# Kernel tuning notes

Hardware: AMD Instinct MI355X
Metric: run time of the kernel (lower is better)

## Reference

```python
import jax, jax.numpy as jnp
import numpy as np

B, T, D = 2, 2048, 1024
N_HEADS, N_KV_HEADS = 16, 4
D_HEAD = D // N_HEADS            # 64
N_GROUPS = N_HEADS // N_KV_HEADS  # 4
ROPE_THETA = 10000.0


def _rope_freqs(t, d_head, theta):
    inv = 1.0 / (theta ** (jnp.arange(0, d_head, 2, dtype=jnp.float32) / d_head))  # (d_head/2,)
    ang = jnp.arange(t, dtype=jnp.float32)[:, None] * inv[None, :]                 # (T, d_head/2)
    return jnp.stack([jnp.cos(ang), jnp.sin(ang)], axis=-1)                        # (T, d_head/2, 2)


def _apply_rope(x, freqs):
    # x: (B, T, H, d_head); freqs: (T, d_head/2, 2) = (cos, sin)
    xr = x.reshape(*x.shape[:-1], -1, 2)          # (B,T,H,d/2,2)
    xre, xim = xr[..., 0], xr[..., 1]
    fre = freqs[None, :, None, :, 0]              # (1,T,1,d/2)
    fim = freqs[None, :, None, :, 1]
    outre = xre * fre - xim * fim
    outim = xre * fim + xim * fre
    return jnp.stack([outre, outim], axis=-1).reshape(x.shape)


def setup_inputs() -> dict:
    key = jax.random.key(0)
    ks = jax.random.split(key, 5)
    x = jax.random.normal(ks[0], (B, T, D), dtype=jnp.float32)
    w_q = jax.random.normal(ks[1], (N_HEADS * D_HEAD, D), dtype=jnp.float32) * 0.02
    w_k = jax.random.normal(ks[2], (N_KV_HEADS * D_HEAD, D), dtype=jnp.float32) * 0.02
    w_v = jax.random.normal(ks[3], (N_KV_HEADS * D_HEAD, D), dtype=jnp.float32) * 0.02
    w_o = jax.random.normal(ks[4], (D, N_HEADS * D_HEAD), dtype=jnp.float32) * 0.02
    rope_freqs = _rope_freqs(T, D_HEAD, ROPE_THETA)
    causal = jnp.tril(jnp.ones((T, T), dtype=bool))
    mask = jnp.where(causal, 0.0, -1e9).astype(jnp.float32)[None, None]  # (1,1,T,T)
    return {"x": x, "rope_freqs": rope_freqs, "mask": mask,
            "w_q": w_q, "w_k": w_k, "w_v": w_v, "w_o": w_o}


def reference(x, rope_freqs, mask, w_q, w_k, w_v, w_o):
    # projections (torch Linear: y = x @ W.T)
    q = jnp.einsum('btd,od->bto', x, w_q).reshape(B, T, N_HEADS, D_HEAD)
    k = jnp.einsum('btd,od->bto', x, w_k).reshape(B, T, N_KV_HEADS, D_HEAD)
    v = jnp.einsum('btd,od->bto', x, w_v).reshape(B, T, N_KV_HEADS, D_HEAD)
    q = _apply_rope(q, rope_freqs)
    k = _apply_rope(k, rope_freqs)
    # GQA: expand KV heads (kv head h -> N_GROUPS contiguous query heads)
    k = jnp.repeat(k, N_GROUPS, axis=2)   # (B,T,H,d)
    v = jnp.repeat(v, N_GROUPS, axis=2)
    q = q.transpose(0, 2, 1, 3)           # (B,H,T,d)
    k = k.transpose(0, 2, 1, 3)
    v = v.transpose(0, 2, 1, 3)
    scale = 1.0 / np.sqrt(D_HEAD).astype(np.float32)
    scores = jnp.einsum('bhqd,bhkd->bhqk', q, k) * scale + mask
    attn = jax.nn.softmax(scores, axis=-1)
    out = jnp.einsum('bhqk,bhkd->bhqd', attn, v)
    out = out.transpose(0, 2, 1, 3).reshape(B, T, N_HEADS * D_HEAD)
    return jnp.einsum('bto,do->btd', out, w_o)
```

## Files before the change

kernel.cpp:

```cpp
#include <hip/hip_runtime.h>
#include <hip/hip_bf16.h>
#include <cstddef>
#include <type_traits>

#define TT   2048
#define NH   16
#define NKV  4
#define DH   64

typedef __bf16 bf16x8 __attribute__((ext_vector_type(8)));
typedef float  f32x4  __attribute__((ext_vector_type(4)));

#if __has_builtin(__builtin_amdgcn_exp2f)
#define EXP2F(x) __builtin_amdgcn_exp2f(x)
#else
#define EXP2F(x) __expf((x) * 0.69314718056f)
#endif

#define QSCALE 0.180336880f

__global__ __launch_bounds__(256)
void cast_kernel(const float* __restrict__ x,  const float* __restrict__ wq,
                 const float* __restrict__ wk, const float* __restrict__ wv,
                 const float* __restrict__ wo,
                 __bf16* __restrict__ xb, __bf16* __restrict__ wqkv,
                 __bf16* __restrict__ wob)
{
    const int g = blockIdx.x * 256 + threadIdx.x;
    const float* src;
    __bf16* dst;
    int off;
    if (g < 1048576)       { src = x;  dst = xb;   off = g; }
    else if (g < 1310720)  { src = wq; dst = wqkv; off = g - 1048576; }
    else if (g < 1376256)  { src = wk; dst = wqkv + 1048576; off = g - 1310720; }
    else if (g < 1441792)  { src = wv; dst = wqkv + 1310720; off = g - 1376256; }
    else                   { src = wo; dst = wob;  off = g - 1441792; }
    const float4 v = *(const float4*)(src + (size_t)off * 4);
    union { __bf16 h[4]; uint2 u; } o;
    o.h[0] = (__bf16)v.x; o.h[1] = (__bf16)v.y;
    o.h[2] = (__bf16)v.z; o.h[3] = (__bf16)v.w;
    *(uint2*)(dst + (size_t)off * 4) = o.u;
}

template<int MODE>
__global__ __launch_bounds__(256, 3)
void mm_kernel(const __bf16* __restrict__ A,
               const __bf16* __restrict__ W,
               const float* __restrict__ rope,
               void* __restrict__ O0, void* __restrict__ O1,
               void* __restrict__ O2)
{
    constexpr int K  = 1024;
    constexpr int NK = K / 32;
    constexpr int NX = (MODE == 0) ? 12 : 8;
    __shared__ __bf16 As[2][64 * 32];
    __shared__ __bf16 Bs[2][128 * 32];

    const int tid  = threadIdx.x;
    const int lane = tid & 63;
    const int wv   = tid >> 6;
    const int quad = lane >> 4;
    const int lc   = lane & 15;

    const int dlin = blockIdx.x + NX * blockIdx.y;
    const int nid  = (dlin & 7) * ((NX * 64) >> 3) + (dlin >> 3);
    const int bx   = nid % NX;
    const int by   = nid / NX;

    const int gm0  = by * 64;
    const int gn0  = bx * 128;
    const int wc0  = wv * 32;

    size_t gaA;  int lsA;
    {
        const int p = tid;
        const int r = p >> 2, q = (p & 3) ^ ((r >> 1) & 3);
        gaA = (size_t)r * K + q * 8;
        lsA = p * 8;
    }
    size_t gaB[2]; int lsB[2];
#pragma unroll
    for (int j = 0; j < 2; j++) {
        const int p = tid + j * 256;
        const int r = p >> 2, q = (p & 3) ^ ((r >> 1) & 3);
        gaB[j] = (size_t)r * K + q * 8;
        lsB[j] = p * 8;
    }
    const __bf16* Ag = A + (size_t)gm0 * K;
    const __bf16* Wg = W + (size_t)gn0 * K;

    auto foff = [&](int row) { return (row * 4 + (quad ^ ((row >> 1) & 3))) * 8; };
    int aoff[4], boff[2];
#pragma unroll
    for (int i = 0; i < 4; i++) aoff[i] = foff(i * 16 + lc);
#pragma unroll
    for (int j = 0; j < 2; j++) boff[j] = foff(wc0 + j * 16 + lc);

    f32x4 acc[4][2];
#pragma unroll
    for (int i = 0; i < 4; i++)
#pragma unroll
        for (int j = 0; j < 2; j++) acc[i][j] = (f32x4){0.f, 0.f, 0.f, 0.f};

    bf16x8 ar[2], br[2][2];

    ar[0] = *(const bf16x8*)(Ag + gaA);
#pragma unroll
    for (int j = 0; j < 2; j++) br[0][j] = *(const bf16x8*)(Wg + gaB[j]);
    *(bf16x8*)&As[0][lsA] = ar[0];
#pragma unroll
    for (int j = 0; j < 2; j++) *(bf16x8*)&Bs[0][lsB[j]] = br[0][j];
    ar[1] = *(const bf16x8*)(Ag + gaA + 32);
#pragma unroll
    for (int j = 0; j < 2; j++) br[1][j] = *(const bf16x8*)(Wg + gaB[j] + 32);
    ar[0] = *(const bf16x8*)(Ag + gaA + 64);
#pragma unroll
    for (int j = 0; j < 2; j++) br[0][j] = *(const bf16x8*)(Wg + gaB[j] + 64);
    __syncthreads();

    auto step = [&](int kt, auto pc) {
        constexpr int P = decltype(pc)::value;
        constexpr int Q = 1 - P;
        bf16x8 af[4], bfr[2];
#pragma unroll
        for (int i = 0; i < 4; i++) af[i]  = *(const bf16x8*)&As[P][aoff[i]];
#pragma unroll
        for (int j = 0; j < 2; j++) bfr[j] = *(const bf16x8*)&Bs[P][boff[j]];
        if (kt + 1 < NK) {
            *(bf16x8*)&As[Q][lsA] = ar[Q];
#pragma unroll
            for (int j = 0; j < 2; j++) *(bf16x8*)&Bs[Q][lsB[j]] = br[Q][j];
        }
#pragma unroll
        for (int i = 0; i < 4; i++)
#pragma unroll
            for (int j = 0; j < 2; j++)
                acc[i][j] = __builtin_amdgcn_mfma_f32_16x16x32_bf16(
                    af[i], bfr[j], acc[i][j], 0, 0, 0);
        if (kt + 3 < NK) {
            const int kb = (kt + 3) * 32;
            ar[Q] = *(const bf16x8*)(Ag + gaA + kb);
#pragma unroll
            for (int j = 0; j < 2; j++) br[Q][j] = *(const bf16x8*)(Wg + gaB[j] + kb);
        }
        if (kt + 1 < NK) __syncthreads();
    };
    for (int kt = 0; kt < NK; kt += 2) {
        step(kt,     std::integral_constant<int, 0>{});
        step(kt + 1, std::integral_constant<int, 1>{});
    }

    if (MODE == 0) {
        __bf16* Qo = (__bf16*)O0;
        __bf16* Ko = (__bf16*)O1;
        __bf16* Vo = (__bf16*)O2;
        const int region = (gn0 < 1024) ? 0 : (gn0 < 1280) ? 1 : 2;
#pragma unroll
        for (int i = 0; i < 4; i++) {
#pragma unroll
            for (int r = 0; r < 4; r++) {
                const int grow = gm0 + i * 16 + quad * 4 + r;
                const int b = grow >> 11, t = grow & 2047;
                const float* rrow = rope + t * 64;
#pragma unroll
                for (int j = 0; j < 2; j++) {
                    const float v = acc[i][j][r];
                    const float partner = __shfl_xor(v, 1, 64);
                    const int col = gn0 + wc0 + j * 16 + lc;
                    if (region == 0) {
                        const int h = col >> 6, d = col & 63;
                        const float2 cs = *(const float2*)(rrow + (d >> 1) * 2);
                        const float out = v * cs.x + partner * ((d & 1) ? cs.y : -cs.y);
                        Qo[((size_t)(b * NH + h) * TT + t) * DH + d] = (__bf16)(out * QSCALE);
                    } else if (region == 1) {
                        const int ck = col - 1024;
                        const int kh = ck >> 6, d = ck & 63;
                        const float2 cs = *(const float2*)(rrow + (d >> 1) * 2);
                        const float out = v * cs.x + partner * ((d & 1) ? cs.y : -cs.y);
                        Ko[((size_t)(b * NKV + kh) * TT + t) * DH + d] = (__bf16)out;
                    } else {
                        const int cv = col - 1280;
                        const int kh = cv >> 6, d = cv & 63;
                        Vo[((size_t)(b * NKV + kh) * DH + d) * TT + t] = (__bf16)v;
                    }
                }
            }
        }
    } else {
        float* Of = (float*)O0;
#pragma unroll
        for (int i = 0; i < 4; i++)
#pragma unroll
            for (int r = 0; r < 4; r++) {
                const int grow = gm0 + i * 16 + quad * 4 + r;
#pragma unroll
                for (int j = 0; j < 2; j++)
                    Of[(size_t)grow * 1024 + gn0 + wc0 + j * 16 + lc] = acc[i][j][r];
            }
    }
}

__global__ __launch_bounds__(128, 2)
void attn_kernel(const __bf16* __restrict__ Q,
                 const __bf16* __restrict__ K,
                 const __bf16* __restrict__ Vt,
                 __bf16* __restrict__ O)
{
    __shared__ __bf16 Ks[64 * 64];
    __shared__ __bf16 Vs[64 * 64];
    __shared__ __bf16 Ps[2][32][72];

    const int tid  = threadIdx.x;
    const int lane = tid & 63;
    const int wv   = tid >> 6;
    const int quad = lane >> 4;
    const int lc   = lane & 15;

    const int a   = blockIdx.x & 31;
    const int rep = blockIdx.x >> 5;
    const int qt  = ((rep >> 3) & 1) ? (31 - a) : a;
    const int b   = rep >> 4;
    const int h   = rep & 15;
    const int kh  = h >> 2;
    const int nk  = qt + 1;

    const __bf16* Kg = K  + (size_t)(b * NKV + kh) * TT * DH;
    const __bf16* Vg = Vt + (size_t)(b * NKV + kh) * DH * TT;

    bf16x8 qb[2][2];
#pragma unroll
    for (int u = 0; u < 2; u++) {
        const __bf16* qp = Q + ((size_t)(b * NH + h) * TT
                                + qt * 64 + wv * 32 + u * 16 + lc) * DH;
        qb[u][0] = *(const bf16x8*)(qp + quad * 8);
        qb[u][1] = *(const bf16x8*)(qp + 32 + quad * 8);
    }

    int koff[4], voff[4], lsl[4];
#pragma unroll
    for (int j = 0; j < 4; j++) {
        const int p  = tid + j * 128;
        const int r  = p >> 3;
        const int qs = (p & 7) ^ (r & 7);
        koff[j] = r * DH + qs * 8;
        voff[j] = r * TT + qs * 8;
        lsl[j]  = p * 8;
    }

    int foff[4][2];
#pragma unroll
    for (int g = 0; g < 4; g++)
#pragma unroll
        for (int c = 0; c < 2; c++)
            foff[g][c] = ((g * 16 + lc) * 8 + ((c * 4 + quad) ^ (lc & 7))) * 8;

    float l_s[2] = {0.f, 0.f};
    f32x4 oacc[2][4];
#pragma unroll
    for (int u = 0; u < 2; u++)
#pragma unroll
        for (int g = 0; g < 4; g++) oacc[u][g] = (f32x4){0.f, 0.f, 0.f, 0.f};

    bf16x8 kr[4], vr[4];
    auto load_regs = [&](int kt) {
        const __bf16* kp = Kg + (size_t)kt * 64 * DH;
        const __bf16* vp = Vg + (size_t)kt * 64;
#pragma unroll
        for (int j = 0; j < 4; j++) {
            kr[j] = *(const bf16x8*)(kp + koff[j]);
            vr[j] = *(const bf16x8*)(vp + voff[j]);
        }
    };
    auto store_lds = [&]() {
#pragma unroll
        for (int j = 0; j < 4; j++) {
            *(bf16x8*)&Ks[lsl[j]] = kr[j];
            *(bf16x8*)&Vs[lsl[j]] = vr[j];
        }
    };

    load_regs(0);
    store_lds();
    if (nk > 1) load_regs(1);
    __syncthreads();

    for (int kt = 0; kt < nk; kt++) {
        bf16x8 ka[4][2];
#pragma unroll
        for (int g = 0; g < 4; g++) {
            ka[g][0] = *(const bf16x8*)&Ks[foff[g][0]];
            ka[g][1] = *(const bf16x8*)&Ks[foff[g][1]];
        }

        const int Dbase = qt * 64 + wv * 32 - kt * 64;

        f32x4 s[2][4];
#pragma unroll
        for (int u = 0; u < 2; u++)
#pragma unroll
            for (int g = 0; g < 4; g++) {
                f32x4 z = (f32x4){0.f, 0.f, 0.f, 0.f};
                z = __builtin_amdgcn_mfma_f32_16x16x32_bf16(ka[g][0], qb[u][0], z, 0, 0, 0);
                z = __builtin_amdgcn_mfma_f32_16x16x32_bf16(ka[g][1], qb[u][1], z, 0, 0, 0);
                s[u][g] = z;
            }

#pragma unroll
        for (int u = 0; u < 2; u++) {
            const int D = Dbase + u * 16;
            if (D < 63) {
                const int thr = D + lc;
#pragma unroll
                for (int g = 0; g < 4; g++)
#pragma unroll
                    for (int r = 0; r < 4; r++)
                        if (g * 16 + quad * 4 + r > thr) s[u][g][r] = -1e30f;
            }
        }

#pragma unroll
        for (int u = 0; u < 2; u++) {
            float rs = 0.f;
#pragma unroll
            for (int g = 0; g < 4; g++) {
#pragma unroll
                for (int r = 0; r < 4; r++) {
                    s[u][g][r] = EXP2F(s[u][g][r]);
                    rs += s[u][g][r];
                }
                union { __bf16 hh[4]; uint2 uu; } pk;
                pk.hh[0] = (__bf16)s[u][g][0]; pk.hh[1] = (__bf16)s[u][g][1];
                pk.hh[2] = (__bf16)s[u][g][2]; pk.hh[3] = (__bf16)s[u][g][3];
                *(uint2*)&Ps[wv][u * 16 + lc][g * 16 + quad * 4] = pk.uu;
            }
            l_s[u] += rs;
        }

        bf16x8 va[4][2];
#pragma unroll
        for (int g = 0; g < 4; g++) {
            va[g][0] = *(const bf16x8*)&Vs[foff[g][0]];
            va[g][1] = *(const bf16x8*)&Vs[foff[g][1]];
        }

#pragma unroll
        for (int u = 0; u < 2; u++) {
            const bf16x8 pb0 = *(const bf16x8*)&Ps[wv][u * 16 + lc][quad * 8];
            const bf16x8 pb1 = *(const bf16x8*)&Ps[wv][u * 16 + lc][32 + quad * 8];
#pragma unroll
            for (int g = 0; g < 4; g++) {
                oacc[u][g] = __builtin_amdgcn_mfma_f32_16x16x32_bf16(va[g][0], pb0, oacc[u][g], 0, 0, 0);
                oacc[u][g] = __builtin_amdgcn_mfma_f32_16x16x32_bf16(va[g][1], pb1, oacc[u][g], 0, 0, 0);
            }
        }

        if (kt + 1 < nk) {
            __syncthreads();
            store_lds();
            if (kt + 2 < nk) load_regs(kt + 2);
            __syncthreads();
        }
    }

#pragma unroll
    for (int u = 0; u < 2; u++) {
        float l = l_s[u];
        l += __shfl_xor(l, 16, 64);
        l += __shfl_xor(l, 32, 64);
        const float inv = 1.f / l;
        const int t = qt * 64 + wv * 32 + u * 16 + lc;
        __bf16* op = O + (size_t)(b * TT + t) * (NH * DH) + h * DH;
#pragma unroll
        for (int g = 0; g < 4; g++) {
            union { __bf16 hh[4]; uint2 uu; } pk;
            pk.hh[0] = (__bf16)(oacc[u][g][0] * inv);
            pk.hh[1] = (__bf16)(oacc[u][g][1] * inv);
            pk.hh[2] = (__bf16)(oacc[u][g][2] * inv);
            pk.hh[3] = (__bf16)(oacc[u][g][3] * inv);
            *(uint2*)(op + g * 16 + quad * 4) = pk.uu;
        }
    }
}

extern "C" void kernel_launch(void* const* d_in, const int* in_sizes, int n_in,
                              void* d_out, int out_size, void* d_ws, size_t ws_size,
                              hipStream_t stream)
{
    const float* x    = (const float*)d_in[0];
    const float* rope = (const float*)d_in[1];
    const float* w_q  = (const float*)d_in[3];
    const float* w_k  = (const float*)d_in[4];
    const float* w_v  = (const float*)d_in[5];
    const float* w_o  = (const float*)d_in[6];
    float* out = (float*)d_out;

    char* ws = (char*)d_ws;
    __bf16* Qb   = (__bf16*)(ws);
    __bf16* Kb   = (__bf16*)(ws + (8  << 20));
    __bf16* Vtb  = (__bf16*)(ws + (10 << 20));
    __bf16* AOb  = (__bf16*)(ws + (12 << 20));
    __bf16* xb   = (__bf16*)(ws + (20 << 20));
    __bf16* Wqkv = (__bf16*)(ws + (28 << 20));
    __bf16* Wob  = (__bf16*)(ws + (31 << 20));

    cast_kernel<<<6656, dim3(256), 0, stream>>>(x, w_q, w_k, w_v, w_o,
                                                xb, Wqkv, Wob);

    dim3 g1(12, 64);
    mm_kernel<0><<<g1, dim3(256), 0, stream>>>(xb, Wqkv, rope,
                                               (void*)Qb, (void*)Kb, (void*)Vtb);

    attn_kernel<<<1024, dim3(128), 0, stream>>>(Qb, Kb, Vtb, AOb);

    dim3 g3(8, 64);
    mm_kernel<1><<<g3, dim3(256), 0, stream>>>(AOb, Wob, rope,
                                               (void*)out, nullptr, nullptr);
}
```

Before: 173.1 us.

## Split attention query tile across four waves with 16 rows each, add setprio

The attention kernel now runs 256 threads per block, with four wavefronts each handling 16 query rows instead of two wavefronts handling 32. This halves per-wave register use and the per-thread K/V tile loads, raising occupancy and latency hiding. s_setprio is also placed around the MFMA sections so the matrix-core phases get scheduling priority. The trade-off is that each K/V tile in LDS is reused across fewer rows per wave, and more waves contend at the block barriers.

After: 176.7 us. 2.0% more time.

```diff
diff --git a/kernel.cpp b/kernel.cpp
--- a/kernel.cpp
+++ b/kernel.cpp
@@ -200,7 +200,7 @@
     }
 }
 
-__global__ __launch_bounds__(128, 2)
+__global__ __launch_bounds__(256, 4)
 void attn_kernel(const __bf16* __restrict__ Q,
                  const __bf16* __restrict__ K,
                  const __bf16* __restrict__ Vt,
@@ -208,7 +208,7 @@
 {
     __shared__ __bf16 Ks[64 * 64];
     __shared__ __bf16 Vs[64 * 64];
-    __shared__ __bf16 Ps[2][32][72];
+    __shared__ __bf16 Ps[4][16][72];
 
     const int tid  = threadIdx.x;
     const int lane = tid & 63;
@@ -227,19 +227,18 @@
     const __bf16* Kg = K  + (size_t)(b * NKV + kh) * TT * DH;
     const __bf16* Vg = Vt + (size_t)(b * NKV + kh) * DH * TT;
 
-    bf16x8 qb[2][2];
-#pragma unroll
-    for (int u = 0; u < 2; u++) {
+    bf16x8 qb[2];
+    {
         const __bf16* qp = Q + ((size_t)(b * NH + h) * TT
-                                + qt * 64 + wv * 32 + u * 16 + lc) * DH;
-        qb[u][0] = *(const bf16x8*)(qp + quad * 8);
-        qb[u][1] = *(const bf16x8*)(qp + 32 + quad * 8);
-    }
-
-    int koff[4], voff[4], lsl[4];
-#pragma unroll
-    for (int j = 0; j < 4; j++) {
-        const int p  = tid + j * 128;
+                                + qt * 64 + wv * 16 + lc) * DH;
+        qb[0] = *(const bf16x8*)(qp + quad * 8);
+        qb[1] = *(const bf16x8*)(qp + 32 + quad * 8);
+    }
+
+    int koff[2], voff[2], lsl[2];
+#pragma unroll
+    for (int j = 0; j < 2; j++) {
+        const int p  = tid + j * 256;
         const int r  = p >> 3;
         const int qs = (p & 7) ^ (r & 7);
         koff[j] = r * DH + qs * 8;
@@ -254,26 +253,24 @@
         for (int c = 0; c < 2; c++)
             foff[g][c] = ((g * 16 + lc) * 8 + ((c * 4 + quad) ^ (lc & 7))) * 8;
 
-    float l_s[2] = {0.f, 0.f};
-    f32x4 oacc[2][4];
-#pragma unroll
-    for (int u = 0; u < 2; u++)
-#pragma unroll
-        for (int g = 0; g < 4; g++) oacc[u][g] = (f32x4){0.f, 0.f, 0.f, 0.f};
-
-    bf16x8 kr[4], vr[4];
+    float l_s = 0.f;
+    f32x4 oacc[4];
+#pragma unroll
+    for (int g = 0; g < 4; g++) oacc[g] = (f32x4){0.f, 0.f, 0.f, 0.f};
+
+    bf16x8 kr[2], vr[2];
     auto load_regs = [&](int kt) {
         const __bf16* kp = Kg + (size_t)kt * 64 * DH;
         const __bf16* vp = Vg + (size_t)kt * 64;
 #pragma unroll
-        for (int j = 0; j < 4; j++) {
+        for (int j = 0; j < 2; j++) {
             kr[j] = *(const bf16x8*)(kp + koff[j]);
             vr[j] = *(const bf16x8*)(vp + voff[j]);
         }
     };
     auto store_lds = [&]() {
 #pragma unroll
-        for (int j = 0; j < 4; j++) {
+        for (int j = 0; j < 2; j++) {
             *(bf16x8*)&Ks[lsl[j]] = kr[j];
             *(bf16x8*)&Vs[lsl[j]] = vr[j];
         }
@@ -292,49 +289,42 @@
             ka[g][1] = *(const bf16x8*)&Ks[foff[g][1]];
         }
 
-        const int Dbase = qt * 64 + wv * 32 - kt * 64;
-
-        f32x4 s[2][4];
-#pragma unroll
-        for (int u = 0; u < 2; u++)
-#pragma unroll
-            for (int g = 0; g < 4; g++) {
-                f32x4 z = (f32x4){0.f, 0.f, 0.f, 0.f};
-                z = __builtin_amdgcn_mfma_f32_16x16x32_bf16(ka[g][0], qb[u][0], z, 0, 0, 0);
-                z = __builtin_amdgcn_mfma_f32_16x16x32_bf16(ka[g][1], qb[u][1], z, 0, 0, 0);
-                s[u][g] = z;
+        const int D = qt * 64 + wv * 16 - kt * 64;
+
+        f32x4 s[4];
+        __builtin_amdgcn_s_setprio(1);
+#pragma unroll
+        for (int g = 0; g < 4; g++) {
+            f32x4 z = (f32x4){0.f, 0.f, 0.f, 0.f};
+            z = __builtin_amdgcn_mfma_f32_16x16x32_bf16(ka[g][0], qb[0], z, 0, 0, 0);
+            z = __builtin_amdgcn_mfma_f32_16x16x32_bf16(ka[g][1], qb[1], z, 0, 0, 0);
+            s[g] = z;
+        }
+        __builtin_amdgcn_s_setprio(0);
+
+        if (D < 63) {
+            const int thr = D + lc;
+#pragma unroll
+            for (int g = 0; g < 4; g++)
+#pragma unroll
+                for (int r = 0; r < 4; r++)
+                    if (g * 16 + quad * 4 + r > thr) s[g][r] = -1e30f;
+        }
+
+        float rs = 0.f;
+#pragma unroll
+        for (int g = 0; g < 4; g++) {
+#pragma unroll
+            for (int r = 0; r < 4; r++) {
+                s[g][r] = EXP2F(s[g][r]);
+                rs += s[g][r];
             }
-
-#pragma unroll
-        for (int u = 0; u < 2; u++) {
-            const int D = Dbase + u * 16;
-            if (D < 63) {
-                const int thr = D + lc;
-#pragma unroll
-                for (int g = 0; g < 4; g++)
-#pragma unroll
-                    for (int r = 0; r < 4; r++)
-                        if (g * 16 + quad * 4 + r > thr) s[u][g][r] = -1e30f;
-            }
-        }
-
-#pragma unroll
-        for (int u = 0; u < 2; u++) {
-            float rs = 0.f;
-#pragma unroll
-            for (int g = 0; g < 4; g++) {
-#pragma unroll
-                for (int r = 0; r < 4; r++) {
-                    s[u][g][r] = EXP2F(s[u][g][r]);
-                    rs += s[u][g][r];
-                }
-                union { __bf16 hh[4]; uint2 uu; } pk;
-                pk.hh[0] = (__bf16)s[u][g][0]; pk.hh[1] = (__bf16)s[u][g][1];
-                pk.hh[2] = (__bf16)s[u][g][2]; pk.hh[3] = (__bf16)s[u][g][3];
-                *(uint2*)&Ps[wv][u * 16 + lc][g * 16 + quad * 4] = pk.uu;
-            }
-            l_s[u] += rs;
-        }
+            union { __bf16 hh[4]; uint2 uu; } pk;
+            pk.hh[0] = (__bf16)s[g][0]; pk.hh[1] = (__bf16)s[g][1];
+            pk.hh[2] = (__bf16)s[g][2]; pk.hh[3] = (__bf16)s[g][3];
+            *(uint2*)&Ps[wv][lc][g * 16 + quad * 4] = pk.uu;
+        }
+        l_s += rs;
 
         bf16x8 va[4][2];
 #pragma unroll
@@ -343,16 +333,15 @@
             va[g][1] = *(const bf16x8*)&Vs[foff[g][1]];
         }
 
-#pragma unroll
-        for (int u = 0; u < 2; u++) {
-            const bf16x8 pb0 = *(const bf16x8*)&Ps[wv][u * 16 + lc][quad * 8];
-            const bf16x8 pb1 = *(const bf16x8*)&Ps[wv][u * 16 + lc][32 + quad * 8];
-#pragma unroll
-            for (int g = 0; g < 4; g++) {
-                oacc[u][g] = __builtin_amdgcn_mfma_f32_16x16x32_bf16(va[g][0], pb0, oacc[u][g], 0, 0, 0);
-                oacc[u][g] = __builtin_amdgcn_mfma_f32_16x16x32_bf16(va[g][1], pb1, oacc[u][g], 0, 0, 0);
-            }
-        }
+        const bf16x8 pb0 = *(const bf16x8*)&Ps[wv][lc][quad * 8];
+        const bf16x8 pb1 = *(const bf16x8*)&Ps[wv][lc][32 + quad * 8];
+        __builtin_amdgcn_s_setprio(1);
+#pragma unroll
+        for (int g = 0; g < 4; g++) {
+            oacc[g] = __builtin_amdgcn_mfma_f32_16x16x32_bf16(va[g][0], pb0, oacc[g], 0, 0, 0);
+            oacc[g] = __builtin_amdgcn_mfma_f32_16x16x32_bf16(va[g][1], pb1, oacc[g], 0, 0, 0);
+        }
+        __builtin_amdgcn_s_setprio(0);
 
         if (kt + 1 < nk) {
             __syncthreads();
@@ -362,21 +351,20 @@
         }
     }
 
-#pragma unroll
-    for (int u = 0; u < 2; u++) {
-        float l = l_s[u];
+    {
+        float l = l_s;
         l += __shfl_xor(l, 16, 64);
         l += __shfl_xor(l, 32, 64);
         const float inv = 1.f / l;
-        const int t = qt * 64 + wv * 32 + u * 16 + lc;
+        const int t = qt * 64 + wv * 16 + lc;
         __bf16* op = O + (size_t)(b * TT + t) * (NH * DH) + h * DH;
 #pragma unroll
         for (int g = 0; g < 4; g++) {
             union { __bf16 hh[4]; uint2 uu; } pk;
-            pk.hh[0] = (__bf16)(oacc[u][g][0] * inv);
-            pk.hh[1] = (__bf16)(oacc[u][g][1] * inv);
-            pk.hh[2] = (__bf16)(oacc[u][g][2] * inv);
-            pk.hh[3] = (__bf16)(oacc[u][g][3] * inv);
+            pk.hh[0] = (__bf16)(oacc[g][0] * inv);
+            pk.hh[1] = (__bf16)(oacc[g][1] * inv);
+            pk.hh[2] = (__bf16)(oacc[g][2] * inv);
+            pk.hh[3] = (__bf16)(oacc[g][3] * inv);
             *(uint2*)(op + g * 16 + quad * 4) = pk.uu;
         }
     }
@@ -410,7 +398,7 @@
     mm_kernel<0><<<g1, dim3(256), 0, stream>>>(xb, Wqkv, rope,
                                                (void*)Qb, (void*)Kb, (void*)Vtb);
 
-    attn_kernel<<<1024, dim3(128), 0, stream>>>(Qb, Kb, Vtb, AOb);
+    attn_kernel<<<1024, dim3(256), 0, stream>>>(Qb, Kb, Vtb, AOb);
 
     dim3 g3(8, 64);
     mm_kernel<1><<<g3, dim3(256), 0, stream>>>(AOb, Wob, rope,
```
